# Optimization experiments

Measured on AMD Instinct MI355X. Metric: run time of the kernel, lower is better.

Reference implementation:

```python
import jax, jax.numpy as jnp
import numpy as np

M = 7          # window size
SHIFT = 3      # window_size // 2 (shift=True)
NUM_HEADS = 4


def _relative_position_index(m):
    coords = np.stack(np.meshgrid(np.arange(m), np.arange(m), indexing='ij')).reshape(2, -1)
    rel = (coords[:, :, None] - coords[:, None, :]).transpose(1, 2, 0).copy()  # (N,N,2)
    rel[..., 0] += m - 1
    rel[..., 1] += m - 1
    rel[..., 0] *= 2 * m - 1
    return rel.sum(-1).astype(np.int32)  # (N,N)


def _shift_attn_mask(H, W, m, s):
    img = np.zeros((H, W), np.float32)
    cnt = 0
    for hs in (slice(0, -m), slice(-m, -s), slice(-s, None)):
        for ws in (slice(0, -m), slice(-m, -s), slice(-s, None)):
            img[hs, ws] = cnt
            cnt += 1
    mw = img.reshape(H // m, m, W // m, m).transpose(0, 2, 1, 3).reshape(-1, m * m)  # (nW, N)
    diff = mw[:, None, :] - mw[:, :, None]
    return np.where(diff != 0, np.float32(-100.0), np.float32(0.0))  # (nW, N, N)


def setup_inputs():
    key = jax.random.key(0)
    k0, k1, k2, k3 = jax.random.split(key, 4)
    B, C, H, W = 32, 128, 112, 112
    h = NUM_HEADS
    x = jax.random.normal(k0, (B, C, H, W), jnp.float32)
    norm_w = jnp.ones((C,), jnp.float32)
    norm_b = jnp.zeros((C,), jnp.float32)
    qkv_w = jax.random.normal(k1, (3 * C, C), jnp.float32) * 0.02
    qkv_b = jnp.zeros((3 * C,), jnp.float32)
    proj_w = jax.random.normal(k2, (C, C), jnp.float32) * 0.02
    proj_b = jnp.zeros((C,), jnp.float32)
    bias_table = jax.random.normal(k3, ((2 * M - 1) ** 2, h), jnp.float32) * 0.02
    rel_index = jnp.asarray(_relative_position_index(M))
    attn_mask = jnp.asarray(_shift_attn_mask(H, W, M, SHIFT))
    return dict(x=x, norm_w=norm_w, norm_b=norm_b, qkv_w=qkv_w, qkv_b=qkv_b,
                proj_w=proj_w, proj_b=proj_b, bias_table=bias_table,
                rel_index=rel_index, attn_mask=attn_mask)


def reference(x, norm_w, norm_b, qkv_w, qkv_b, proj_w, proj_b, bias_table, rel_index, attn_mask):
    B, C, H, W = x.shape
    h = bias_table.shape[1]
    d = C // h
    N = M * M
    nH, nW = H // M, W // M

    xp = jnp.transpose(x, (0, 2, 3, 1))  # (B,H,W,C)
    shortcut = xp
    mu = xp.mean(-1, keepdims=True)
    var = ((xp - mu) ** 2).mean(-1, keepdims=True)
    xn = (xp - mu) / jnp.sqrt(var + 1e-5) * norm_w + norm_b

    xn = jnp.roll(xn, (-SHIFT, -SHIFT), (1, 2))  # cyclic shift

    # window partition -> (B*nH*nW, N, C)
    w = xn.reshape(B, nH, M, nW, M, C).transpose((0, 1, 3, 2, 4, 5)).reshape(-1, N, C)

    qkv = w @ qkv_w.T + qkv_b  # (B_, N, 3C)
    qkv = qkv.reshape(-1, N, 3, h, d).transpose((2, 0, 3, 1, 4))  # (3, B_, h, N, d)
    q, k, v = qkv[0], qkv[1], qkv[2]

    attn = jnp.einsum('bhnd,bhmd->bhnm', q, k) * (d ** -0.5)  # (B_, h, N, N)
    bias = bias_table[rel_index.reshape(-1)].reshape(N, N, h).transpose((2, 0, 1))  # (h,N,N)
    attn = attn + bias[None]

    nWnd = attn_mask.shape[0]  # number of windows per image
    attn = attn.reshape(B, nWnd, h, N, N) + attn_mask[None, :, None]
    attn = attn.reshape(-1, h, N, N)

    p = jax.nn.softmax(attn, axis=-1)
    o = jnp.einsum('bhnm,bhmd->bhnd', p, v).transpose((0, 2, 1, 3)).reshape(-1, N, C)
    o = o @ proj_w.T + proj_b

    # window reverse -> (B,H,W,C)
    o = o.reshape(B, nH, nW, M, M, C).transpose((0, 1, 3, 2, 4, 5)).reshape(B, H, W, C)
    o = jnp.roll(o, (SHIFT, SHIFT), (1, 2))  # reverse shift

    return jnp.transpose(shortcut + o, (0, 3, 1, 2))  # (B,C,H,W)
```

## Files before the change

### kernel.cpp

```cpp
#include <hip/hip_runtime.h>
#include <hip/hip_bf16.h>

typedef __attribute__((ext_vector_type(8))) short bf16x8;
typedef __attribute__((ext_vector_type(4))) float f32x4;
typedef __attribute__((ext_vector_type(8))) unsigned short ushort8;

__device__ __forceinline__ float bf2f(unsigned short u) {
  union { unsigned int i; float f; } v; v.i = ((unsigned int)u) << 16; return v.f;
}
__device__ __forceinline__ unsigned short f2bf(float f) {
  __hip_bfloat16 h = __float2bfloat16(f);
  unsigned short u; __builtin_memcpy(&u, &h, 2); return u;
}

__global__ void k_prep(const float* __restrict__ qkvw, const float* __restrict__ projw,
                       unsigned short* __restrict__ qkvw_bf,
                       unsigned short* __restrict__ projw_bf) {
  int t = blockIdx.x * 256 + threadIdx.x;
  int i = t * 4;
  const float* src;
  unsigned short* dst;
  int idx;
  if (i < 49152) { src = qkvw; dst = qkvw_bf; idx = i; }
  else           { src = projw; dst = projw_bf; idx = i - 49152; }
  float4 v = *(const float4*)(src + idx);
  union { unsigned short u[4]; uint2 v2; } o;
  o.u[0] = f2bf(v.x); o.u[1] = f2bf(v.y); o.u[2] = f2bf(v.z); o.u[3] = f2bf(v.w);
  *(uint2*)(dst + idx) = o.v2;
}

__global__ void k_bias(const float* __restrict__ bt,
                       const int* __restrict__ ri,
                       float* __restrict__ b2d) {
  int t = blockIdx.x * 256 + threadIdx.x;
  if (t < 9604) {
    int hq = t / 2401;
    int rc = t - hq * 2401;
    b2d[t] = bt[ri[rc] * 4 + hq];
  }
}

__global__ __launch_bounds__(256, 4) void k_ln(const float* __restrict__ x,
                                               const float* __restrict__ nw,
                                               const float* __restrict__ nb,
                                               unsigned short* __restrict__ xw) {
  int p = blockIdx.x * 256 + threadIdx.x;
  int b = p / 12544;
  int r = p - b * 12544;
  int hh = r / 112;
  int wp = r - hh * 112;
  const float* bx = x + (size_t)b * 1605632 + r;

  float sum = 0.f, ss = 0.f;
  #pragma unroll 16
  for (int c = 0; c < 128; ++c) {
    float v = bx[(size_t)c * 12544];
    sum += v; ss += v * v;
  }
  float mu = sum * 0.0078125f;
  float var = ss * 0.0078125f - mu * mu;
  float rstd = rsqrtf(var + 1e-5f);

  int h2 = hh + 109; if (h2 >= 112) h2 -= 112;
  int w2 = wp + 109; if (w2 >= 112) w2 -= 112;
  int wh = h2 / 7, ii = h2 - wh * 7;
  int ww = w2 / 7, jj = w2 - ww * 7;
  int winl = (b * 16 + wh) * 16 + ww;
  unsigned short* dst = xw + ((size_t)winl * 49 + ii * 7 + jj) * 128;

  #pragma unroll
  for (int g = 0; g < 4; ++g) {
    unsigned int pk[16];
    #pragma unroll
    for (int q = 0; q < 16; ++q) {
      int c = g * 32 + 2 * q;
      float v0 = bx[(size_t)c * 12544];
      float v1 = bx[(size_t)(c + 1) * 12544];
      float y0 = (v0 - mu) * rstd * nw[c]     + nb[c];
      float y1 = (v1 - mu) * rstd * nw[c + 1] + nb[c + 1];
      pk[q] = (unsigned int)f2bf(y0) | ((unsigned int)f2bf(y1) << 16);
    }
    uint4* d4 = (uint4*)(dst + g * 32);
    #pragma unroll
    for (int k = 0; k < 4; ++k)
      d4[k] = make_uint4(pk[4 * k], pk[4 * k + 1], pk[4 * k + 2], pk[4 * k + 3]);
  }
}

__global__ __launch_bounds__(256, 2) void k_attn(
    const unsigned short* __restrict__ xw,
    const unsigned short* __restrict__ qkvw,
    const float* __restrict__ qkvb,
    const unsigned short* __restrict__ projw,
    const float* __restrict__ projb,
    const float* __restrict__ b2d,
    const float* __restrict__ amask,
    unsigned short* __restrict__ yw) {
  __shared__ __attribute__((aligned(16))) char smem[59392];
  const int tid  = threadIdx.x;
  const int lane = tid & 63;
  const int h    = tid >> 6;
  const int m15  = lane & 15;
  const int quad = lane >> 4;
  const int win  = blockIdx.x;
  const int b    = win >> 8;
  const int wrem = win & 255;
  const int wh   = wrem >> 4;
  const int ww   = wrem & 15;
  const f32x4 fz = {0.f, 0.f, 0.f, 0.f};

  {
    const uint4* gsrc = (const uint4*)(xw + (size_t)win * 6272);
    #pragma unroll
    for (int it = 0; it < 4; ++it) {
      int cc = tid + it * 256;
      int row = cc >> 4, col = cc & 15;
      uint4 v = make_uint4(0u, 0u, 0u, 0u);
      if (cc < 784) v = gsrc[cc];
      *(uint4*)(smem + row * 272 + col * 16) = v;
    }
  }
  __syncthreads();

  bf16x8 xf[4][4];
  #pragma unroll
  for (int mt = 0; mt < 4; ++mt)
    #pragma unroll
    for (int kt = 0; kt < 4; ++kt)
      xf[mt][kt] = *(const bf16x8*)(smem + (mt * 16 + m15) * 272 + kt * 64 + quad * 16);
  __syncthreads();

  char* const hb  = smem + h * 14848;
  char* const qpb = hb;
  char* const kpb = hb + 5120;
  char* const vpb = hb + 10240;

  #pragma unroll
  for (int g = 0; g < 3; ++g) {
    #pragma unroll
    for (int sp = 0; sp < 2; ++sp) {
      int nt = g * 8 + 2 * h + sp;
      int f = nt * 16 + m15;
      bf16x8 wfr[4];
      #pragma unroll
      for (int kt = 0; kt < 4; ++kt)
        wfr[kt] = *(const bf16x8*)(qkvw + f * 128 + kt * 32 + quad * 8);
      float bias = qkvb[f];
      int dsub = sp * 16 + m15;
      #pragma unroll
      for (int mt = 0; mt < 4; ++mt) {
        f32x4 acc = fz;
        #pragma unroll
        for (int kt = 0; kt < 4; ++kt)
          acc = __builtin_amdgcn_mfma_f32_16x16x32_bf16(xf[mt][kt], wfr[kt], acc, 0, 0, 0);
        #pragma unroll
        for (int rr = 0; rr < 4; ++rr) {
          int token = mt * 16 + quad * 4 + rr;
          unsigned short val = f2bf(acc[rr] + bias);
          if (g == 0)      *(unsigned short*)(qpb + token * 80 + dsub * 2) = val;
          else if (g == 1) *(unsigned short*)(kpb + token * 80 + dsub * 2) = val;
          else             *(unsigned short*)(vpb + dsub * 144 + token * 2) = val;
        }
      }
    }
  }

  bf16x8 qf[4], kf[4];
  #pragma unroll
  for (int t = 0; t < 4; ++t) {
    qf[t] = *(const bf16x8*)(qpb + (t * 16 + m15) * 80 + quad * 16);
    kf[t] = *(const bf16x8*)(kpb + (t * 16 + m15) * 80 + quad * 16);
  }
  f32x4 sacc[4][4];
  #pragma unroll
  for (int mt = 0; mt < 4; ++mt)
    #pragma unroll
    for (int nt = 0; nt < 4; ++nt)
      sacc[mt][nt] = __builtin_amdgcn_mfma_f32_16x16x32_bf16(qf[mt], kf[nt], fz, 0, 0, 0);

  const float* bp = b2d + h * 2401;
  const float* mp = amask + wrem * 2401;
  #pragma unroll
  for (int mt = 0; mt < 4; ++mt) {
    #pragma unroll
    for (int rr = 0; rr < 4; ++rr) {
      int row = mt * 16 + quad * 4 + rr;
      int rb = row * 49;
      float sv[4];
      #pragma unroll
      for (int nt = 0; nt < 4; ++nt) {
        int col = nt * 16 + m15;
        float s = -1e30f;
        if (row < 49 && col < 49)
          s = sacc[mt][nt][rr] * 0.17677669529663687f + bp[rb + col] + mp[rb + col];
        sv[nt] = s;
      }
      float mx = fmaxf(fmaxf(sv[0], sv[1]), fmaxf(sv[2], sv[3]));
      mx = fmaxf(mx, __shfl_xor(mx, 1));
      mx = fmaxf(mx, __shfl_xor(mx, 2));
      mx = fmaxf(mx, __shfl_xor(mx, 4));
      mx = fmaxf(mx, __shfl_xor(mx, 8));
      float pv[4]; float sum = 0.f;
      #pragma unroll
      for (int nt = 0; nt < 4; ++nt) { pv[nt] = __expf(sv[nt] - mx); sum += pv[nt]; }
      sum += __shfl_xor(sum, 1);
      sum += __shfl_xor(sum, 2);
      sum += __shfl_xor(sum, 4);
      sum += __shfl_xor(sum, 8);
      float rinv = 1.0f / sum;
      #pragma unroll
      for (int nt = 0; nt < 4; ++nt)
        *(unsigned short*)(qpb + row * 144 + (nt * 16 + m15) * 2) = f2bf(pv[nt] * rinv);
    }
  }

  f32x4 oacc[4][2];
  #pragma unroll
  for (int mt = 0; mt < 4; ++mt) {
    #pragma unroll
    for (int nt = 0; nt < 2; ++nt) {
      f32x4 acc = fz;
      #pragma unroll
      for (int kt = 0; kt < 2; ++kt) {
        bf16x8 pf = *(const bf16x8*)(qpb + (mt * 16 + m15) * 144 + kt * 64 + quad * 16);
        bf16x8 vf = *(const bf16x8*)(vpb + (nt * 16 + m15) * 144 + kt * 64 + quad * 16);
        acc = __builtin_amdgcn_mfma_f32_16x16x32_bf16(pf, vf, acc, 0, 0, 0);
      }
      oacc[mt][nt] = acc;
    }
  }
  #pragma unroll
  for (int mt = 0; mt < 4; ++mt)
    #pragma unroll
    for (int nt = 0; nt < 2; ++nt)
      #pragma unroll
      for (int rr = 0; rr < 4; ++rr) {
        int token = mt * 16 + quad * 4 + rr;
        *(unsigned short*)(qpb + token * 80 + (nt * 16 + m15) * 2) = f2bf(oacc[mt][nt][rr]);
      }
  __syncthreads();

  bf16x8 of[4][4];
  #pragma unroll
  for (int mt = 0; mt < 4; ++mt)
    #pragma unroll
    for (int kt = 0; kt < 4; ++kt)
      of[mt][kt] = *(const bf16x8*)(smem + kt * 14848 + (mt * 16 + m15) * 80 + quad * 16);

  const size_t obase = (size_t)b * 1605632;
  #pragma unroll
  for (int sp = 0; sp < 2; ++sp) {
    int cout = (2 * h + sp) * 16 + m15;
    bf16x8 wf[4];
    #pragma unroll
    for (int kt = 0; kt < 4; ++kt)
      wf[kt] = *(const bf16x8*)(projw + cout * 128 + kt * 32 + quad * 8);
    float pb = projb[cout];
    #pragma unroll
    for (int mt = 0; mt < 4; ++mt) {
      f32x4 acc = fz;
      #pragma unroll
      for (int kt = 0; kt < 4; ++kt)
        acc = __builtin_amdgcn_mfma_f32_16x16x32_bf16(of[mt][kt], wf[kt], acc, 0, 0, 0);
      #pragma unroll
      for (int rr = 0; rr < 4; ++rr) {
        int token = mt * 16 + quad * 4 + rr;
        if (token < 49) {
          int ii = token / 7, jj = token - ii * 7;
          int gh = wh * 7 + ii + 3; if (gh >= 112) gh -= 112;
          int gw = ww * 7 + jj + 3; if (gw >= 112) gw -= 112;
          yw[obase + ((size_t)(gh * 112 + gw)) * 128 + cout] = f2bf(acc[rr] + pb);
        }
      }
    }
  }
}

__global__ __launch_bounds__(256) void k_out(const unsigned short* __restrict__ yws,
                                             const float* __restrict__ x,
                                             float* __restrict__ out) {
  __shared__ unsigned short T[128 * 128];
  int tid = threadIdx.x;
  int bid = blockIdx.x;
  int b = bid / 112;
  int hh = bid - b * 112;
  const unsigned short* src = yws + (size_t)(b * 112 + hh) * 14336;
  #pragma unroll
  for (int it = 0; it < 7; ++it) {
    int cc = tid + it * 256;
    int w = cc >> 4, c8 = (cc & 15) * 8;
    ushort8 v = *(const ushort8*)(src + w * 128 + c8);
    #pragma unroll
    for (int k = 0; k < 8; ++k) T[(c8 + k) * 128 + w] = v[k];
  }
  __syncthreads();
  int c = tid >> 1, half = tid & 1;
  size_t rowoff = ((size_t)(b * 128 + c) * 112 + hh) * 112;
  const float* xr = x + rowoff;
  float* outr = out + rowoff;
  #pragma unroll
  for (int s2 = 0; s2 < 7; ++s2) {
    int w = half * 56 + s2 * 8;
    ushort8 yv = *(const ushort8*)(T + c * 128 + w);
    float4 xa = *(const float4*)(xr + w);
    float4 xb = *(const float4*)(xr + w + 4);
    float4 oa, ob;
    oa.x = bf2f(yv[0]) + xa.x; oa.y = bf2f(yv[1]) + xa.y;
    oa.z = bf2f(yv[2]) + xa.z; oa.w = bf2f(yv[3]) + xa.w;
    ob.x = bf2f(yv[4]) + xb.x; ob.y = bf2f(yv[5]) + xb.y;
    ob.z = bf2f(yv[6]) + xb.z; ob.w = bf2f(yv[7]) + xb.w;
    *(float4*)(outr + w) = oa;
    *(float4*)(outr + w + 4) = ob;
  }
}

extern "C" void kernel_launch(void* const* d_in, const int* in_sizes, int n_in,
                              void* d_out, int out_size, void* d_ws, size_t ws_size,
                              hipStream_t stream) {
  const float* x     = (const float*)d_in[0];
  const float* nw    = (const float*)d_in[1];
  const float* nb    = (const float*)d_in[2];
  const float* qkvw  = (const float*)d_in[3];
  const float* qkvb  = (const float*)d_in[4];
  const float* projw = (const float*)d_in[5];
  const float* projb = (const float*)d_in[6];
  const float* bt    = (const float*)d_in[7];
  const int*   ri    = (const int*)d_in[8];
  const float* am    = (const float*)d_in[9];

  unsigned short* xw   = (unsigned short*)d_ws;
  unsigned short* yws  = (unsigned short*)((char*)d_ws + 102760448);
  float*          b2d  = (float*)((char*)d_ws + 205520896);
  unsigned short* qwbf = (unsigned short*)((char*)d_ws + 205559312);
  unsigned short* pwbf = (unsigned short*)((char*)d_ws + 205657616);
  float* out = (float*)d_out;

  k_prep<<<64,   256, 0, stream>>>(qkvw, projw, qwbf, pwbf);
  k_bias<<<38,   256, 0, stream>>>(bt, ri, b2d);
  k_ln  <<<1568, 256, 0, stream>>>(x, nw, nb, xw);
  k_attn<<<8192, 256, 0, stream>>>(xw, qwbf, qkvb, pwbf, projb, b2d, am, yws);
  k_out <<<3584, 256, 0, stream>>>(yws, x, out);
}
```

Measured before the change: 815.9 us.

## Swizzle LDS layouts, transpose MFMA operands, pad bias/mask, cache LN inputs

Reworks the attention kernel's shared-memory layout with XOR swizzles and smaller buffers to cut bank conflicts, and raises occupancy to 3 blocks per CU. It swaps MFMA operand order so each lane holds contiguous outputs, which allows packed 8-byte LDS and global stores and float4 bias/mask loads. Bias and mask are pre-padded to 64x64 tables with -1e30 in the padded entries, so the softmax needs no bounds checks. LayerNorm keeps all 128 channel values in registers instead of reading x twice, and the output transpose uses a padded 16-byte-chunk LDS layout. The extra mask precompute kernel and the higher register pressure from the larger live state are the costs.

```diff
diff --git a/kernel.cpp b/kernel.cpp
--- a/kernel.cpp
+++ b/kernel.cpp
@@ -31,16 +31,27 @@
 
 __global__ void k_bias(const float* __restrict__ bt,
                        const int* __restrict__ ri,
-                       float* __restrict__ b2d) {
+                       float* __restrict__ bp) {
   int t = blockIdx.x * 256 + threadIdx.x;
-  if (t < 9604) {
-    int hq = t / 2401;
-    int rc = t - hq * 2401;
-    b2d[t] = bt[ri[rc] * 4 + hq];
-  }
-}
-
-__global__ __launch_bounds__(256, 4) void k_ln(const float* __restrict__ x,
+  int hq = t >> 12;
+  int q  = (t >> 6) & 63;
+  int k  = t & 63;
+  float v = -1e30f;
+  if (q < 49 && k < 49) v = bt[ri[q * 49 + k] * 4 + hq];
+  bp[t] = v;
+}
+
+__global__ void k_mask(const float* __restrict__ am, float* __restrict__ mp) {
+  int t = blockIdx.x * 256 + threadIdx.x;
+  int w = t >> 12;
+  int q = (t >> 6) & 63;
+  int k = t & 63;
+  float v = -1e30f;
+  if (q < 49 && k < 49) v = am[w * 2401 + q * 49 + k];
+  mp[t] = v;
+}
+
+__global__ __launch_bounds__(256, 3) void k_ln(const float* __restrict__ x,
                                                const float* __restrict__ nw,
                                                const float* __restrict__ nb,
                                                unsigned short* __restrict__ xw) {
@@ -51,14 +62,18 @@
   int wp = r - hh * 112;
   const float* bx = x + (size_t)b * 1605632 + r;
 
-  float sum = 0.f, ss = 0.f;
-  #pragma unroll 16
-  for (int c = 0; c < 128; ++c) {
-    float v = bx[(size_t)c * 12544];
-    sum += v; ss += v * v;
-  }
-  float mu = sum * 0.0078125f;
-  float var = ss * 0.0078125f - mu * mu;
+  float v[128];
+  float s0 = 0.f, s1 = 0.f, q0 = 0.f, q1 = 0.f;
+  #pragma unroll
+  for (int c = 0; c < 128; c += 2) {
+    float a = bx[(size_t)c * 12544];
+    float bb = bx[(size_t)(c + 1) * 12544];
+    v[c] = a; v[c + 1] = bb;
+    s0 += a; q0 += a * a;
+    s1 += bb; q1 += bb * bb;
+  }
+  float mu = (s0 + s1) * 0.0078125f;
+  float var = (q0 + q1) * 0.0078125f - mu * mu;
   float rstd = rsqrtf(var + 1e-5f);
 
   int h2 = hh + 109; if (h2 >= 112) h2 -= 112;
@@ -74,10 +89,8 @@
     #pragma unroll
     for (int q = 0; q < 16; ++q) {
       int c = g * 32 + 2 * q;
-      float v0 = bx[(size_t)c * 12544];
-      float v1 = bx[(size_t)(c + 1) * 12544];
-      float y0 = (v0 - mu) * rstd * nw[c]     + nb[c];
-      float y1 = (v1 - mu) * rstd * nw[c + 1] + nb[c + 1];
+      float y0 = (v[c] - mu) * rstd * nw[c]         + nb[c];
+      float y1 = (v[c + 1] - mu) * rstd * nw[c + 1] + nb[c + 1];
       pk[q] = (unsigned int)f2bf(y0) | ((unsigned int)f2bf(y1) << 16);
     }
     uint4* d4 = (uint4*)(dst + g * 32);
@@ -87,16 +100,16 @@
   }
 }
 
-__global__ __launch_bounds__(256, 2) void k_attn(
+__global__ __launch_bounds__(256, 3) void k_attn(
     const unsigned short* __restrict__ xw,
     const unsigned short* __restrict__ qkvw,
     const float* __restrict__ qkvb,
     const unsigned short* __restrict__ projw,
     const float* __restrict__ projb,
-    const float* __restrict__ b2d,
-    const float* __restrict__ amask,
+    const float* __restrict__ biasp,
+    const float* __restrict__ maskp,
     unsigned short* __restrict__ yw) {
-  __shared__ __attribute__((aligned(16))) char smem[59392];
+  __shared__ __attribute__((aligned(16))) char smem[49152];
   const int tid  = threadIdx.x;
   const int lane = tid & 63;
   const int h    = tid >> 6;
@@ -117,160 +130,191 @@
       int row = cc >> 4, col = cc & 15;
       uint4 v = make_uint4(0u, 0u, 0u, 0u);
       if (cc < 784) v = gsrc[cc];
-      *(uint4*)(smem + row * 272 + col * 16) = v;
+      *(uint4*)(smem + row * 256 + ((col ^ (row & 7)) << 4)) = v;
     }
   }
   __syncthreads();
 
   bf16x8 xf[4][4];
   #pragma unroll
-  for (int mt = 0; mt < 4; ++mt)
+  for (int mt = 0; mt < 4; ++mt) {
+    int row = mt * 16 + m15;
     #pragma unroll
     for (int kt = 0; kt < 4; ++kt)
-      xf[mt][kt] = *(const bf16x8*)(smem + (mt * 16 + m15) * 272 + kt * 64 + quad * 16);
+      xf[mt][kt] = *(const bf16x8*)(smem + row * 256 + (((kt * 4 + quad) ^ (row & 7)) << 4));
+  }
   __syncthreads();
 
-  char* const hb  = smem + h * 14848;
+  char* const hb  = smem + h * 12288;
   char* const qpb = hb;
-  char* const kpb = hb + 5120;
-  char* const vpb = hb + 10240;
-
-  #pragma unroll
-  for (int g = 0; g < 3; ++g) {
+  char* const kpb = hb + 4096;
+  char* const vpb = hb + 8192;
+
+  #pragma unroll
+  for (int g = 0; g < 2; ++g) {
+    char* const dst = g ? kpb : qpb;
     #pragma unroll
     for (int sp = 0; sp < 2; ++sp) {
       int nt = g * 8 + 2 * h + sp;
-      int f = nt * 16 + m15;
       bf16x8 wfr[4];
       #pragma unroll
       for (int kt = 0; kt < 4; ++kt)
-        wfr[kt] = *(const bf16x8*)(qkvw + f * 128 + kt * 32 + quad * 8);
-      float bias = qkvb[f];
-      int dsub = sp * 16 + m15;
+        wfr[kt] = *(const bf16x8*)(qkvw + (nt * 16 + m15) * 128 + kt * 32 + quad * 8);
+      float4 b4 = *(const float4*)(qkvb + nt * 16 + quad * 4);
       #pragma unroll
       for (int mt = 0; mt < 4; ++mt) {
         f32x4 acc = fz;
         #pragma unroll
         for (int kt = 0; kt < 4; ++kt)
-          acc = __builtin_amdgcn_mfma_f32_16x16x32_bf16(xf[mt][kt], wfr[kt], acc, 0, 0, 0);
-        #pragma unroll
-        for (int rr = 0; rr < 4; ++rr) {
-          int token = mt * 16 + quad * 4 + rr;
-          unsigned short val = f2bf(acc[rr] + bias);
-          if (g == 0)      *(unsigned short*)(qpb + token * 80 + dsub * 2) = val;
-          else if (g == 1) *(unsigned short*)(kpb + token * 80 + dsub * 2) = val;
-          else             *(unsigned short*)(vpb + dsub * 144 + token * 2) = val;
-        }
+          acc = __builtin_amdgcn_mfma_f32_16x16x32_bf16(wfr[kt], xf[mt][kt], acc, 0, 0, 0);
+        int row = mt * 16 + m15;
+        union { unsigned short u[4]; uint2 v2; } o;
+        o.u[0] = f2bf(acc[0] + b4.x); o.u[1] = f2bf(acc[1] + b4.y);
+        o.u[2] = f2bf(acc[2] + b4.z); o.u[3] = f2bf(acc[3] + b4.w);
+        int chunk = sp * 2 + (quad >> 1);
+        *(uint2*)(dst + row * 64 + ((chunk ^ ((row >> 1) & 3)) << 4) + (quad & 1) * 8) = o.v2;
       }
     }
   }
-
-  bf16x8 qf[4], kf[4];
-  #pragma unroll
-  for (int t = 0; t < 4; ++t) {
-    qf[t] = *(const bf16x8*)(qpb + (t * 16 + m15) * 80 + quad * 16);
-    kf[t] = *(const bf16x8*)(kpb + (t * 16 + m15) * 80 + quad * 16);
-  }
-  f32x4 sacc[4][4];
-  #pragma unroll
-  for (int mt = 0; mt < 4; ++mt)
-    #pragma unroll
-    for (int nt = 0; nt < 4; ++nt)
-      sacc[mt][nt] = __builtin_amdgcn_mfma_f32_16x16x32_bf16(qf[mt], kf[nt], fz, 0, 0, 0);
-
-  const float* bp = b2d + h * 2401;
-  const float* mp = amask + wrem * 2401;
-  #pragma unroll
-  for (int mt = 0; mt < 4; ++mt) {
-    #pragma unroll
-    for (int rr = 0; rr < 4; ++rr) {
-      int row = mt * 16 + quad * 4 + rr;
-      int rb = row * 49;
-      float sv[4];
-      #pragma unroll
-      for (int nt = 0; nt < 4; ++nt) {
-        int col = nt * 16 + m15;
-        float s = -1e30f;
-        if (row < 49 && col < 49)
-          s = sacc[mt][nt][rr] * 0.17677669529663687f + bp[rb + col] + mp[rb + col];
-        sv[nt] = s;
-      }
-      float mx = fmaxf(fmaxf(sv[0], sv[1]), fmaxf(sv[2], sv[3]));
-      mx = fmaxf(mx, __shfl_xor(mx, 1));
-      mx = fmaxf(mx, __shfl_xor(mx, 2));
-      mx = fmaxf(mx, __shfl_xor(mx, 4));
-      mx = fmaxf(mx, __shfl_xor(mx, 8));
-      float pv[4]; float sum = 0.f;
-      #pragma unroll
-      for (int nt = 0; nt < 4; ++nt) { pv[nt] = __expf(sv[nt] - mx); sum += pv[nt]; }
-      sum += __shfl_xor(sum, 1);
-      sum += __shfl_xor(sum, 2);
-      sum += __shfl_xor(sum, 4);
-      sum += __shfl_xor(sum, 8);
-      float rinv = 1.0f / sum;
-      #pragma unroll
-      for (int nt = 0; nt < 4; ++nt)
-        *(unsigned short*)(qpb + row * 144 + (nt * 16 + m15) * 2) = f2bf(pv[nt] * rinv);
-    }
-  }
-
-  f32x4 oacc[4][2];
-  #pragma unroll
-  for (int mt = 0; mt < 4; ++mt) {
-    #pragma unroll
-    for (int nt = 0; nt < 2; ++nt) {
-      f32x4 acc = fz;
-      #pragma unroll
-      for (int kt = 0; kt < 2; ++kt) {
-        bf16x8 pf = *(const bf16x8*)(qpb + (mt * 16 + m15) * 144 + kt * 64 + quad * 16);
-        bf16x8 vf = *(const bf16x8*)(vpb + (nt * 16 + m15) * 144 + kt * 64 + quad * 16);
-        acc = __builtin_amdgcn_mfma_f32_16x16x32_bf16(pf, vf, acc, 0, 0, 0);
-      }
-      oacc[mt][nt] = acc;
-    }
-  }
-  #pragma unroll
-  for (int mt = 0; mt < 4; ++mt)
-    #pragma unroll
-    for (int nt = 0; nt < 2; ++nt)
-      #pragma unroll
-      for (int rr = 0; rr < 4; ++rr) {
-        int token = mt * 16 + quad * 4 + rr;
-        *(unsigned short*)(qpb + token * 80 + (nt * 16 + m15) * 2) = f2bf(oacc[mt][nt][rr]);
-      }
-  __syncthreads();
-
-  bf16x8 of[4][4];
-  #pragma unroll
-  for (int mt = 0; mt < 4; ++mt)
+  #pragma unroll
+  for (int sp = 0; sp < 2; ++sp) {
+    int nt = 16 + 2 * h + sp;
+    bf16x8 wfr[4];
     #pragma unroll
     for (int kt = 0; kt < 4; ++kt)
-      of[mt][kt] = *(const bf16x8*)(smem + kt * 14848 + (mt * 16 + m15) * 80 + quad * 16);
-
-  const size_t obase = (size_t)b * 1605632;
-  #pragma unroll
-  for (int sp = 0; sp < 2; ++sp) {
-    int cout = (2 * h + sp) * 16 + m15;
-    bf16x8 wf[4];
-    #pragma unroll
-    for (int kt = 0; kt < 4; ++kt)
-      wf[kt] = *(const bf16x8*)(projw + cout * 128 + kt * 32 + quad * 8);
-    float pb = projb[cout];
+      wfr[kt] = *(const bf16x8*)(qkvw + (nt * 16 + m15) * 128 + kt * 32 + quad * 8);
+    float bias = qkvb[nt * 16 + m15];
+    int dsub = sp * 16 + m15;
     #pragma unroll
     for (int mt = 0; mt < 4; ++mt) {
       f32x4 acc = fz;
       #pragma unroll
       for (int kt = 0; kt < 4; ++kt)
-        acc = __builtin_amdgcn_mfma_f32_16x16x32_bf16(of[mt][kt], wf[kt], acc, 0, 0, 0);
-      #pragma unroll
-      for (int rr = 0; rr < 4; ++rr) {
-        int token = mt * 16 + quad * 4 + rr;
-        if (token < 49) {
-          int ii = token / 7, jj = token - ii * 7;
-          int gh = wh * 7 + ii + 3; if (gh >= 112) gh -= 112;
-          int gw = ww * 7 + jj + 3; if (gw >= 112) gw -= 112;
-          yw[obase + ((size_t)(gh * 112 + gw)) * 128 + cout] = f2bf(acc[rr] + pb);
-        }
+        acc = __builtin_amdgcn_mfma_f32_16x16x32_bf16(xf[mt][kt], wfr[kt], acc, 0, 0, 0);
+      union { unsigned short u[4]; uint2 v2; } o;
+      #pragma unroll
+      for (int rr = 0; rr < 4; ++rr) o.u[rr] = f2bf(acc[rr] + bias);
+      int chunk = mt * 2 + (quad >> 1);
+      *(uint2*)(vpb + dsub * 128 + ((chunk ^ (dsub & 7)) << 4) + (quad & 1) * 8) = o.v2;
+    }
+  }
+
+  bf16x8 qf[4], kf[4];
+  #pragma unroll
+  for (int t = 0; t < 4; ++t) {
+    int row = t * 16 + m15;
+    int sw = ((row >> 1) & 3) << 4;
+    qf[t] = *(const bf16x8*)(qpb + row * 64 + ((quad << 4) ^ sw));
+    kf[t] = *(const bf16x8*)(kpb + row * 64 + ((quad << 4) ^ sw));
+  }
+  f32x4 st[4][4];
+  #pragma unroll
+  for (int nt = 0; nt < 4; ++nt)
+    #pragma unroll
+    for (int mt = 0; mt < 4; ++mt)
+      st[nt][mt] = __builtin_amdgcn_mfma_f32_16x16x32_bf16(kf[nt], qf[mt], fz, 0, 0, 0);
+
+  const float* bp = biasp + h * 4096;
+  const float* mp = maskp + wrem * 4096;
+  #pragma unroll
+  for (int mt = 0; mt < 4; ++mt) {
+    int q = mt * 16 + m15;
+    float sv[16];
+    #pragma unroll
+    for (int nt = 0; nt < 4; ++nt) {
+      float4 bb = *(const float4*)(bp + q * 64 + nt * 16 + quad * 4);
+      float4 mm = *(const float4*)(mp + q * 64 + nt * 16 + quad * 4);
+      sv[nt * 4 + 0] = st[nt][mt][0] * 0.17677669529663687f + bb.x + mm.x;
+      sv[nt * 4 + 1] = st[nt][mt][1] * 0.17677669529663687f + bb.y + mm.y;
+      sv[nt * 4 + 2] = st[nt][mt][2] * 0.17677669529663687f + bb.z + mm.z;
+      sv[nt * 4 + 3] = st[nt][mt][3] * 0.17677669529663687f + bb.w + mm.w;
+    }
+    float mx = sv[0];
+    #pragma unroll
+    for (int j = 1; j < 16; ++j) mx = fmaxf(mx, sv[j]);
+    mx = fmaxf(mx, __shfl_xor(mx, 16));
+    mx = fmaxf(mx, __shfl_xor(mx, 32));
+    float sum = 0.f;
+    #pragma unroll
+    for (int j = 0; j < 16; ++j) { sv[j] = __expf(sv[j] - mx); sum += sv[j]; }
+    sum += __shfl_xor(sum, 16);
+    sum += __shfl_xor(sum, 32);
+    float rinv = 1.0f / sum;
+    #pragma unroll
+    for (int nt = 0; nt < 4; ++nt) {
+      union { unsigned short u[4]; uint2 v2; } o;
+      #pragma unroll
+      for (int rr = 0; rr < 4; ++rr) o.u[rr] = f2bf(sv[nt * 4 + rr] * rinv);
+      int chunk = nt * 2 + (quad >> 1);
+      *(uint2*)(qpb + q * 128 + ((chunk ^ (m15 & 7)) << 4) + (quad & 1) * 8) = o.v2;
+    }
+  }
+
+  #pragma unroll
+  for (int tt = 0; tt < 4; ++tt) {
+    bf16x8 pf[2];
+    #pragma unroll
+    for (int kt = 0; kt < 2; ++kt) {
+      int row = tt * 16 + m15;
+      pf[kt] = *(const bf16x8*)(qpb + row * 128 + (((kt * 4 + quad) ^ (m15 & 7)) << 4));
+    }
+    #pragma unroll
+    for (int dt = 0; dt < 2; ++dt) {
+      f32x4 acc = fz;
+      #pragma unroll
+      for (int kt = 0; kt < 2; ++kt) {
+        bf16x8 vf = *(const bf16x8*)(vpb + (dt * 16 + m15) * 128 + (((kt * 4 + quad) ^ (m15 & 7)) << 4));
+        acc = __builtin_amdgcn_mfma_f32_16x16x32_bf16(vf, pf[kt], acc, 0, 0, 0);
+      }
+      int row = tt * 16 + m15;
+      union { unsigned short u[4]; uint2 v2; } o;
+      #pragma unroll
+      for (int rr = 0; rr < 4; ++rr) o.u[rr] = f2bf(acc[rr]);
+      int chunk = dt * 2 + (quad >> 1);
+      *(uint2*)(qpb + row * 64 + ((chunk ^ ((row >> 1) & 3)) << 4) + (quad & 1) * 8) = o.v2;
+    }
+  }
+  __syncthreads();
+
+  bf16x8 of[4][4];
+  #pragma unroll
+  for (int mt = 0; mt < 4; ++mt) {
+    int row = mt * 16 + m15;
+    int sw = ((row >> 1) & 3) << 4;
+    #pragma unroll
+    for (int kt = 0; kt < 4; ++kt)
+      of[mt][kt] = *(const bf16x8*)(smem + kt * 12288 + row * 64 + ((quad << 4) ^ sw));
+  }
+  int pixo[4];
+  #pragma unroll
+  for (int mt = 0; mt < 4; ++mt) {
+    int token = mt * 16 + m15;
+    int ii = token / 7, jj = token - ii * 7;
+    int gh = wh * 7 + ii + 3; if (gh >= 112) gh -= 112;
+    int gw = ww * 7 + jj + 3; if (gw >= 112) gw -= 112;
+    pixo[mt] = gh * 112 + gw;
+  }
+  const size_t obase = (size_t)b * 1605632;
+  #pragma unroll
+  for (int sp = 0; sp < 2; ++sp) {
+    int ct = 2 * h + sp;
+    bf16x8 wf[4];
+    #pragma unroll
+    for (int kt = 0; kt < 4; ++kt)
+      wf[kt] = *(const bf16x8*)(projw + (ct * 16 + m15) * 128 + kt * 32 + quad * 8);
+    float4 pb4 = *(const float4*)(projb + ct * 16 + quad * 4);
+    #pragma unroll
+    for (int mt = 0; mt < 4; ++mt) {
+      f32x4 acc = fz;
+      #pragma unroll
+      for (int kt = 0; kt < 4; ++kt)
+        acc = __builtin_amdgcn_mfma_f32_16x16x32_bf16(wf[kt], of[mt][kt], acc, 0, 0, 0);
+      int token = mt * 16 + m15;
+      if (token < 49) {
+        union { unsigned short u[4]; uint2 v2; } o;
+        o.u[0] = f2bf(acc[0] + pb4.x); o.u[1] = f2bf(acc[1] + pb4.y);
+        o.u[2] = f2bf(acc[2] + pb4.z); o.u[3] = f2bf(acc[3] + pb4.w);
+        *(uint2*)(yw + obase + (size_t)pixo[mt] * 128 + ct * 16 + quad * 4) = o.v2;
       }
     }
   }
@@ -279,7 +323,7 @@
 __global__ __launch_bounds__(256) void k_out(const unsigned short* __restrict__ yws,
                                              const float* __restrict__ x,
                                              float* __restrict__ out) {
-  __shared__ unsigned short T[128 * 128];
+  __shared__ __attribute__((aligned(16))) char T[28928];
   int tid = threadIdx.x;
   int bid = blockIdx.x;
   int b = bid / 112;
@@ -288,27 +332,29 @@
   #pragma unroll
   for (int it = 0; it < 7; ++it) {
     int cc = tid + it * 256;
-    int w = cc >> 4, c8 = (cc & 15) * 8;
-    ushort8 v = *(const ushort8*)(src + w * 128 + c8);
-    #pragma unroll
-    for (int k = 0; k < 8; ++k) T[(c8 + k) * 128 + w] = v[k];
+    int w = cc >> 4, ci = cc & 15;
+    *(uint4*)(T + ci * 1808 + w * 16) = *(const uint4*)(src + w * 128 + ci * 8);
   }
   __syncthreads();
   int c = tid >> 1, half = tid & 1;
+  const char* tr = T + (c >> 3) * 1808 + (c & 7) * 2;
   size_t rowoff = ((size_t)(b * 128 + c) * 112 + hh) * 112;
   const float* xr = x + rowoff;
   float* outr = out + rowoff;
   #pragma unroll
   for (int s2 = 0; s2 < 7; ++s2) {
     int w = half * 56 + s2 * 8;
-    ushort8 yv = *(const ushort8*)(T + c * 128 + w);
     float4 xa = *(const float4*)(xr + w);
     float4 xb = *(const float4*)(xr + w + 4);
     float4 oa, ob;
-    oa.x = bf2f(yv[0]) + xa.x; oa.y = bf2f(yv[1]) + xa.y;
-    oa.z = bf2f(yv[2]) + xa.z; oa.w = bf2f(yv[3]) + xa.w;
-    ob.x = bf2f(yv[4]) + xb.x; ob.y = bf2f(yv[5]) + xb.y;
-    ob.z = bf2f(yv[6]) + xb.z; ob.w = bf2f(yv[7]) + xb.w;
+    oa.x = bf2f(*(const unsigned short*)(tr + (w + 0) * 16)) + xa.x;
+    oa.y = bf2f(*(const unsigned short*)(tr + (w + 1) * 16)) + xa.y;
+    oa.z = bf2f(*(const unsigned short*)(tr + (w + 2) * 16)) + xa.z;
+    oa.w = bf2f(*(const unsigned short*)(tr + (w + 3) * 16)) + xa.w;
+    ob.x = bf2f(*(const unsigned short*)(tr + (w + 4) * 16)) + xb.x;
+    ob.y = bf2f(*(const unsigned short*)(tr + (w + 5) * 16)) + xb.y;
+    ob.z = bf2f(*(const unsigned short*)(tr + (w + 6) * 16)) + xb.z;
+    ob.w = bf2f(*(const unsigned short*)(tr + (w + 7) * 16)) + xb.w;
     *(float4*)(outr + w) = oa;
     *(float4*)(outr + w + 4) = ob;
   }
@@ -330,14 +376,16 @@
 
   unsigned short* xw   = (unsigned short*)d_ws;
   unsigned short* yws  = (unsigned short*)((char*)d_ws + 102760448);
-  float*          b2d  = (float*)((char*)d_ws + 205520896);
-  unsigned short* qwbf = (unsigned short*)((char*)d_ws + 205559312);
-  unsigned short* pwbf = (unsigned short*)((char*)d_ws + 205657616);
+  float*          bp   = (float*)((char*)d_ws + 205520896);
+  float*          mp   = (float*)((char*)d_ws + 205586432);
+  unsigned short* qwbf = (unsigned short*)((char*)d_ws + 209780736);
+  unsigned short* pwbf = (unsigned short*)((char*)d_ws + 209879040);
   float* out = (float*)d_out;
 
   k_prep<<<64,   256, 0, stream>>>(qkvw, projw, qwbf, pwbf);
-  k_bias<<<38,   256, 0, stream>>>(bt, ri, b2d);
+  k_bias<<<64,   256, 0, stream>>>(bt, ri, bp);
+  k_mask<<<4096, 256, 0, stream>>>(am, mp);
   k_ln  <<<1568, 256, 0, stream>>>(x, nw, nb, xw);
-  k_attn<<<8192, 256, 0, stream>>>(xw, qwbf, qkvb, pwbf, projb, b2d, am, yws);
+  k_attn<<<8192, 256, 0, stream>>>(xw, qwbf, qkvb, pwbf, projb, bp, mp, yws);
   k_out <<<3584, 256, 0, stream>>>(yws, x, out);
 }
```

Result: slower. 848.9 us (+4.0%).
